# Kernel tuning notes

Hardware: AMD Instinct MI355X
Metric: run time of the kernel (lower is better)

## Reference

```python
import jax, jax.numpy as jnp
import numpy as np

N_NODES = 100000
N_EDGES = 1600000
D_FEAT = 128
HIDDEN = 128
N_CLASSES = 40


def setup_inputs() -> dict:
    key = jax.random.key(0)
    ks = jax.random.split(key, 8)
    s = 1.0 / np.sqrt(HIDDEN)
    return {
        "x": jax.random.normal(ks[0], (N_NODES, D_FEAT), dtype=jnp.float32),
        "edge_index": jax.random.randint(ks[1], (2, N_EDGES), 0, N_NODES, dtype=jnp.int64),
        "w1a": jax.random.normal(ks[2], (D_FEAT, HIDDEN), dtype=jnp.float32) * s,
        "b1a": jnp.zeros((HIDDEN,), dtype=jnp.float32),
        "w1b": jax.random.normal(ks[3], (HIDDEN, HIDDEN), dtype=jnp.float32) * s,
        "b1b": jnp.zeros((HIDDEN,), dtype=jnp.float32),
        "w2a": jax.random.normal(ks[4], (HIDDEN, HIDDEN), dtype=jnp.float32) * s,
        "b2a": jnp.zeros((HIDDEN,), dtype=jnp.float32),
        "w2b": jax.random.normal(ks[5], (HIDDEN, HIDDEN), dtype=jnp.float32) * s,
        "b2b": jnp.zeros((HIDDEN,), dtype=jnp.float32),
        "wfc": jax.random.normal(ks[6], (HIDDEN, N_CLASSES), dtype=jnp.float32) * s,
        "bfc": jnp.zeros((N_CLASSES,), dtype=jnp.float32),
    }


def _gin_conv(x, src, dst, wa, ba, wb, bb):
    # sum-aggregate neighbor features: agg[i] = sum_{(j->i) in E} x[j]
    agg = jax.ops.segment_sum(x[src], dst, num_segments=N_NODES)
    h = x + agg  # eps = 0 (PyG GINConv default)
    h = jax.nn.relu(h @ wa + ba)
    return h @ wb + bb


def reference(x, edge_index, w1a, b1a, w1b, b1b, w2a, b2a, w2b, b2b, wfc, bfc):
    src, dst = edge_index[0], edge_index[1]
    h = jax.nn.relu(_gin_conv(x, src, dst, w1a, b1a, w1b, b1b))
    # dropout is identity at inference
    h = jax.nn.relu(_gin_conv(h, src, dst, w2a, b2a, w2b, b2b))
    logits = h @ wfc + bfc
    return jax.nn.log_softmax(logits, axis=1)
```

## Files before the change

### kernel.cpp

```cpp
#include <hip/hip_runtime.h>
#include <hip/hip_bf16.h>

#define NNODES 100000
#define NEDGES 1600000
#define DF 128
#define NC 40
#define NCP 48
#define NB 196
#define CH 4096
#define MLP_BLOCKS 512
#define MLP_WAVES (MLP_BLOCKS * 4)
#define ZROW NNODES
#define CVT_BLOCKS 6250
#define WPREP_N (4 * 16384 + NCP * 128 + 512 + NC + 512)
#define WPREP_BLOCKS ((WPREP_N + 255) / 256)
#define NEB ((NEDGES + CH - 1) / CH)

typedef __bf16 bf16x8 __attribute__((ext_vector_type(8)));
typedef float f32x4 __attribute__((ext_vector_type(4)));
typedef float f32x2 __attribute__((ext_vector_type(2)));

__device__ __forceinline__ unsigned short f2bf(float f) {
    unsigned int u = __builtin_bit_cast(unsigned int, f);
    u = (u + 0x7FFFu + ((u >> 16) & 1u)) >> 16;
    return (unsigned short)u;
}
__device__ __forceinline__ float bf2f(unsigned short s) {
    unsigned int u = ((unsigned int)s) << 16;
    return __builtin_bit_cast(float, u);
}
__device__ __forceinline__ float bfLo(unsigned int u) {
    return __builtin_bit_cast(float, u << 16);
}
__device__ __forceinline__ float bfHi(unsigned int u) {
    return __builtin_bit_cast(float, u & 0xFFFF0000u);
}
__device__ __forceinline__ f32x2 up2(unsigned int u) {
    return (f32x2){bfLo(u), bfHi(u)};
}

__global__ void k_detect(const unsigned int* __restrict__ ei32,
                         const unsigned int* __restrict__ x32,
                         int* __restrict__ flags,
                         int* __restrict__ binCnt) {
    __shared__ unsigned int rOr[256];
    __shared__ int rCnt[256];
    for (int i = threadIdx.x; i < NB; i += 256) binCnt[i] = 0;
    unsigned int o = 0; int c = 0;
    for (int i = threadIdx.x; i < 1024; i += 256) o |= ei32[2 * i + 1];
    for (int i = threadIdx.x; i < 4096; i += 256) {
        unsigned int e = (x32[i] >> 7) & 0xFFu;
        c += (e >= 100u && e <= 140u) ? 1 : 0;
    }
    rOr[threadIdx.x] = o; rCnt[threadIdx.x] = c;
    __syncthreads();
    for (int s = 128; s; s >>= 1) {
        if ((int)threadIdx.x < s) {
            rOr[threadIdx.x] |= rOr[threadIdx.x + s];
            rCnt[threadIdx.x] += rCnt[threadIdx.x + s];
        }
        __syncthreads();
    }
    if (threadIdx.x == 0) {
        flags[0] = (rOr[0] == 0u) ? 1 : 0;
        flags[1] = (rCnt[0] > 2457) ? 1 : 0;
    }
}

__device__ __forceinline__ int ldIdx(const void* ei, int flag64, int i) {
    return flag64 ? (int)((const long long*)ei)[i] : ((const int*)ei)[i];
}

__global__ __launch_bounds__(256) void k_prep(const void* __restrict__ src,
                                              const void* w1a, const void* w1b,
                                              const void* w2a, const void* w2b,
                                              const void* wfc,
                                              const void* b1a, const void* b1b,
                                              const void* b2a, const void* b2b,
                                              const void* bfc,
                                              const void* __restrict__ ei,
                                              const int* __restrict__ flags,
                                              unsigned short* __restrict__ dst,
                                              unsigned short* __restrict__ wAll,
                                              float* __restrict__ bAll,
                                              unsigned short* __restrict__ pad0,
                                              unsigned short* __restrict__ pad1,
                                              int* __restrict__ binCnt) {
    int bf = flags[1];
    if (blockIdx.x < CVT_BLOCKS) {
        int i = blockIdx.x * 256 + threadIdx.x;
        if (bf) {
            ((uint4*)dst)[i] = ((const uint4*)src)[i];
        } else {
            uint4 a = ((const uint4*)src)[2 * i];
            uint4 b = ((const uint4*)src)[2 * i + 1];
            auto pk = [](unsigned int lo, unsigned int hi) -> unsigned int {
                return ((unsigned int)f2bf(__builtin_bit_cast(float, hi)) << 16) |
                       f2bf(__builtin_bit_cast(float, lo));
            };
            uint4 r;
            r.x = pk(a.x, a.y);
            r.y = pk(a.z, a.w);
            r.z = pk(b.x, b.y);
            r.w = pk(b.z, b.w);
            ((uint4*)dst)[i] = r;
        }
        return;
    }
    if (blockIdx.x >= CVT_BLOCKS + WPREP_BLOCKS) {
        __shared__ int l[NB];
        int t = threadIdx.x;
        int f64 = flags[0];
        for (int i = t; i < NB; i += 256) l[i] = 0;
        __syncthreads();
        int base = (blockIdx.x - CVT_BLOCKS - WPREP_BLOCKS) * CH;
#pragma unroll
        for (int k = 0; k < CH / 256; k++) {
            int e = base + k * 256 + t;
            if (e < NEDGES) atomicAdd(&l[ldIdx(ei, f64, NEDGES + e) >> 9], 1);
        }
        __syncthreads();
        for (int i = t; i < NB; i += 256)
            if (l[i]) atomicAdd(&binCnt[i], l[i]);
        return;
    }
    int idx = (blockIdx.x - CVT_BLOCKS) * 256 + threadIdx.x;
    auto ldf = [&](const void* p, int i) -> float {
        return bf ? bf2f(((const unsigned short*)p)[i]) : ((const float*)p)[i];
    };
    if (idx < 65536) {
        int wi = idx >> 14, r = idx & 16383;
        int n = r >> 7, k = r & 127;
        const void* s = (wi == 0) ? w1a : (wi == 1) ? w1b : (wi == 2) ? w2a : w2b;
        wAll[idx] = f2bf(ldf(s, k * 128 + n));
    } else if (idx < 65536 + NCP * 128) {
        int r = idx - 65536;
        int n = r >> 7, k = r & 127;
        wAll[idx] = (n < NC) ? f2bf(ldf(wfc, k * NC + n)) : (unsigned short)0;
    } else if (idx < 65536 + NCP * 128 + 512 + NC) {
        int r = idx - (65536 + NCP * 128);
        const void* s; int i;
        if (r < 128)      { s = b1a; i = r; }
        else if (r < 256) { s = b1b; i = r - 128; }
        else if (r < 384) { s = b2a; i = r - 256; }
        else if (r < 512) { s = b2b; i = r - 384; }
        else              { s = bfc; i = r - 512; }
        bAll[r] = ldf(s, i);
    } else if (idx < 65536 + NCP * 128 + 512 + NC + 256) {
        pad0[idx - (65536 + NCP * 128 + 512 + NC)] = 0;
    } else if (idx < 65536 + NCP * 128 + 512 + NC + 512) {
        pad1[idx - (65536 + NCP * 128 + 512 + NC + 256)] = 0;
    }
}

__global__ __launch_bounds__(256) void k_binscan(const int* __restrict__ binCnt,
                                                 int* __restrict__ binOfs,
                                                 int* __restrict__ binCur) {
    __shared__ int sh[256];
    int t = threadIdx.x;
    int v = (t < NB) ? binCnt[t] : 0;
    sh[t] = v;
    __syncthreads();
    for (int off = 1; off < 256; off <<= 1) {
        int x = (t >= off) ? sh[t - off] : 0;
        __syncthreads();
        sh[t] += x;
        __syncthreads();
    }
    if (t < NB) {
        binOfs[t + 1] = sh[t];
        binCur[t] = sh[t] - v;
    }
    if (t == 0) binOfs[0] = 0;
}

__global__ __launch_bounds__(256) void k_binscatter(const void* __restrict__ ei,
                                                    const int* __restrict__ flags,
                                                    int* __restrict__ binCur,
                                                    int2* __restrict__ ebin) {
    __shared__ int lcnt[NB], lbase[NB], lofs[NB];
    int t = threadIdx.x;
    int f64 = flags[0];
    for (int i = t; i < NB; i += 256) lcnt[i] = 0;
    __syncthreads();
    int base = blockIdx.x * CH;
    int2 ed[CH / 256];
    int bn[CH / 256];
#pragma unroll
    for (int k = 0; k < CH / 256; k++) {
        int e = base + k * 256 + t;
        if (e < NEDGES) {
            ed[k].x = ldIdx(ei, f64, e);
            ed[k].y = ldIdx(ei, f64, NEDGES + e);
            bn[k] = ed[k].y >> 9;
            atomicAdd(&lcnt[bn[k]], 1);
        } else bn[k] = -1;
    }
    __syncthreads();
    if (t < NB) {
        int c = lcnt[t];
        lbase[t] = c ? atomicAdd(&binCur[t], c) : 0;
        lofs[t] = 0;
    }
    __syncthreads();
#pragma unroll
    for (int k = 0; k < CH / 256; k++) {
        if (bn[k] >= 0) {
            int p = lbase[bn[k]] + atomicAdd(&lofs[bn[k]], 1);
            ebin[p] = ed[k];
        }
    }
}

__global__ __launch_bounds__(256) void k_binfill(const int2* __restrict__ ebin,
                                                 const int* __restrict__ binOfs,
                                                 int* __restrict__ rowptr,
                                                 int* __restrict__ perm) {
    __shared__ int deg[512], lptr[512], ssum[256];
    int b = blockIdx.x, t = threadIdx.x;
    int n0 = b << 9;
    int nn = NNODES - n0; if (nn > 512) nn = 512;
    int e0 = binOfs[b], e1 = binOfs[b + 1];
    deg[t] = 0; deg[t + 256] = 0;
    __syncthreads();
    for (int e = e0 + t; e < e1; e += 256)
        atomicAdd(&deg[ebin[e].y - n0], 1);
    __syncthreads();
    int d0 = deg[2 * t], d1 = deg[2 * t + 1];
    int s = d0 + d1;
    ssum[t] = s;
    __syncthreads();
    for (int off = 1; off < 256; off <<= 1) {
        int x = (t >= off) ? ssum[t - off] : 0;
        __syncthreads();
        ssum[t] += x;
        __syncthreads();
    }
    int ex = ssum[t] - s;
    lptr[2 * t] = ex;
    lptr[2 * t + 1] = ex + d0;
    if (2 * t < nn)     rowptr[n0 + 2 * t] = e0 + ex;
    if (2 * t + 1 < nn) rowptr[n0 + 2 * t + 1] = e0 + ex + d0;
    if (b == NB - 1 && t == 0) rowptr[NNODES] = e1;
    deg[2 * t] = 0; deg[2 * t + 1] = 0;
    __syncthreads();
    for (int e = e0 + t; e < e1; e += 256) {
        int2 ed = ebin[e];
        int d = ed.y - n0;
        int pos = e0 + lptr[d] + atomicAdd(&deg[d], 1);
        perm[pos] = ed.x;
    }
}

__device__ __forceinline__ void accu(f32x2* acc, uint4 u) {
    acc[0] += up2(u.x);
    acc[1] += up2(u.y);
    acc[2] += up2(u.z);
    acc[3] += up2(u.w);
}

template <int S>
__device__ __forceinline__ void gslots(const int* __restrict__ perm, const uint4* __restrict__ F,
                                       int j, int je, int g, int c, f32x2* acc) {
    int pm[S];
#pragma unroll
    for (int k = 0; k < S; k++) pm[k] = perm[j + 4 * k + g];
#pragma unroll
    for (int k = 0; k < S; k++)
        if (j + 4 * k + g >= je) pm[k] = ZROW;
    uint4 u[S];
#pragma unroll
    for (int k = 0; k < S; k++) u[k] = F[pm[k] * 16 + c];
#pragma unroll
    for (int k = 0; k < S; k++) accu(acc, u[k]);
}

__global__ __launch_bounds__(256) void k_gather(const unsigned short* __restrict__ feat,
                                                const unsigned short* __restrict__ x,
                                                const int* __restrict__ rowptr,
                                                const int* __restrict__ perm,
                                                unsigned short* __restrict__ out) {
    int wave = threadIdx.x >> 6, lane = threadIdx.x & 63;
    int i = blockIdx.x * 4 + wave;
    int g = lane >> 4, c = lane & 15;
    const uint4* F = (const uint4*)feat;

    uint4 xv = ((const uint4*)x)[i * 16 + c];
    int jb = rowptr[i], je = rowptr[i + 1];

    f32x2 acc[4];
#pragma unroll
    for (int k = 0; k < 4; k++) acc[k] = (f32x2){0.f, 0.f};

    int j = jb;
    while (je - j > 24) {
        int s0 = perm[j + g], s1 = perm[j + 4 + g];
        int s2 = perm[j + 8 + g], s3 = perm[j + 12 + g];
        uint4 u0 = F[s0 * 16 + c];
        uint4 u1 = F[s1 * 16 + c];
        uint4 u2 = F[s2 * 16 + c];
        uint4 u3 = F[s3 * 16 + c];
        accu(acc, u0); accu(acc, u1); accu(acc, u2); accu(acc, u3);
        j += 16;
    }
    int deg = je - j;
    if (deg > 16)      gslots<6>(perm, F, j, je, g, c, acc);
    else if (deg > 8)  gslots<4>(perm, F, j, je, g, c, acc);
    else if (deg > 0)  gslots<2>(perm, F, j, je, g, c, acc);

#pragma unroll
    for (int k = 0; k < 4; k++) {
        acc[k][0] += __shfl_xor(acc[k][0], 16);
        acc[k][1] += __shfl_xor(acc[k][1], 16);
        acc[k][0] += __shfl_xor(acc[k][0], 32);
        acc[k][1] += __shfl_xor(acc[k][1], 32);
    }

    acc[0] += up2(xv.x);
    acc[1] += up2(xv.y);
    acc[2] += up2(xv.z);
    acc[3] += up2(xv.w);

    if (g == 0) {
        uint4 r;
        r.x = ((unsigned int)f2bf(acc[0][1]) << 16) | f2bf(acc[0][0]);
        r.y = ((unsigned int)f2bf(acc[1][1]) << 16) | f2bf(acc[1][0]);
        r.z = ((unsigned int)f2bf(acc[2][1]) << 16) | f2bf(acc[2][0]);
        r.w = ((unsigned int)f2bf(acc[3][1]) << 16) | f2bf(acc[3][0]);
        ((uint4*)out)[i * 16 + c] = r;
    }
}

template <bool DOFC>
__global__ __launch_bounds__(256, 2) void k_mlp_lds(const unsigned short* __restrict__ A,
                                                    const unsigned short* __restrict__ WaT,
                                                    const float* __restrict__ ba,
                                                    const unsigned short* __restrict__ WbT,
                                                    const float* __restrict__ bb,
                                                    const unsigned short* __restrict__ WfcT,
                                                    const float* __restrict__ bfc,
                                                    const int* __restrict__ flags,
                                                    unsigned short* __restrict__ outH,
                                                    void* __restrict__ outFC) {
    __shared__ __align__(16) unsigned short sWa[16384];
    __shared__ __align__(16) unsigned short sWb[16384];
    __shared__ __align__(16) unsigned short sT[4][2048];

    int wave = threadIdx.x >> 6, lane = threadIdx.x & 63;
    int gw = blockIdx.x * 4 + wave;
    int m = lane & 15, quad = lane >> 4;
    unsigned short* T = sT[wave];

    {
        const uint4* Wa4 = (const uint4*)WaT;
        const uint4* Wb4 = (const uint4*)WbT;
        uint4* sA4 = (uint4*)sWa;
        uint4* sB4 = (uint4*)sWb;
        for (int idx = (int)threadIdx.x; idx < 2048; idx += 256) {
            int n = idx >> 4, kc = idx & 15;
            int d = (n << 4) | (kc ^ (n & 15));
            sA4[d] = Wa4[idx];
            sB4[d] = Wb4[idx];
        }
    }

    float bva[8], bvb[8];
#pragma unroll
    for (int nt = 0; nt < 8; nt++) { bva[nt] = ba[nt * 16 + m]; bvb[nt] = bb[nt * 16 + m]; }

    bf16x8 wf[3][4];
    float fv0 = 0.f, fv1 = 0.f, fv2 = 0.f;
    bool valid2 = (m < 8);
    int obf = 0;
    if (DOFC) {
#pragma unroll
        for (int nt = 0; nt < 3; nt++) {
            const unsigned short* Bf = WfcT + (nt * 16 + m) * DF + quad * 8;
#pragma unroll
            for (int ks = 0; ks < 4; ks++) wf[nt][ks] = *(const bf16x8*)(Bf + ks * 32);
        }
        fv0 = bfc[m]; fv1 = bfc[16 + m];
        fv2 = valid2 ? bfc[32 + m] : 0.f;
        obf = flags[1];
    }
    __syncthreads();

    for (int tile = gw; tile < NNODES / 16; tile += MLP_WAVES) {
        int r0 = tile * 16;
        const unsigned short* Ab = A + (r0 + m) * DF + quad * 8;
        bf16x8 a[4];
#pragma unroll
        for (int ks = 0; ks < 4; ks++) a[ks] = *(const bf16x8*)(Ab + ks * 32);

        f32x4 acc[8];
#pragma unroll
        for (int nt = 0; nt < 8; nt++) acc[nt] = (f32x4){0.f, 0.f, 0.f, 0.f};
#pragma unroll
        for (int nt = 0; nt < 8; nt++) {
#pragma unroll
            for (int ks = 0; ks < 4; ks++) {
                bf16x8 w = *(const bf16x8*)&sWa[((nt * 16 + m) << 7) | ((((ks << 2) + quad) ^ m) << 3)];
                acc[nt] = __builtin_amdgcn_mfma_f32_16x16x32_bf16(a[ks], w, acc[nt], 0, 0, 0);
            }
        }

#pragma unroll
        for (int nt = 0; nt < 8; nt++)
#pragma unroll
            for (int reg = 0; reg < 4; reg++) {
                float v = acc[nt][reg] + bva[nt];
                if (v < 0.f) v = 0.f;
                int row = quad * 4 + reg, col = nt * 16 + m;
                T[(row << 7) | ((((col >> 3) ^ row) & 15) << 3) | (col & 7)] = f2bf(v);
            }

        bf16x8 a2[4];
#pragma unroll
        for (int ks = 0; ks < 4; ks++)
            a2[ks] = *(const bf16x8*)&T[(m << 7) | ((((ks << 2) + quad) ^ m) << 3)];
#pragma unroll
        for (int nt = 0; nt < 8; nt++) acc[nt] = (f32x4){0.f, 0.f, 0.f, 0.f};
#pragma unroll
        for (int nt = 0; nt < 8; nt++) {
#pragma unroll
            for (int ks = 0; ks < 4; ks++) {
                bf16x8 w = *(const bf16x8*)&sWb[((nt * 16 + m) << 7) | ((((ks << 2) + quad) ^ m) << 3)];
                acc[nt] = __builtin_amdgcn_mfma_f32_16x16x32_bf16(a2[ks], w, acc[nt], 0, 0, 0);
            }
        }

        if (!DOFC) {
#pragma unroll
            for (int nt = 0; nt < 8; nt++)
#pragma unroll
                for (int reg = 0; reg < 4; reg++) {
                    float v = acc[nt][reg] + bvb[nt];
                    if (v < 0.f) v = 0.f;
                    int row = quad * 4 + reg, col = nt * 16 + m;
                    T[(row << 7) | ((((col >> 3) ^ row) & 15) << 3) | (col & 7)] = f2bf(v);
                }
            int r2 = lane >> 3, c8 = lane & 7;
            const uint4* T4 = (const uint4*)T;
            uint4* O4 = (uint4*)(outH + (size_t)r0 * DF);
#pragma unroll
            for (int half = 0; half < 2; half++) {
                int row = r2 + half * 8;
#pragma unroll
                for (int lin = 0; lin < 2; lin++) {
                    int ch = c8 + lin * 8;
                    uint4 v = T4[(row << 4) | (ch ^ row)];
                    O4[row * 16 + ch] = v;
                }
            }
        } else {
#pragma unroll
            for (int nt = 0; nt < 8; nt++)
#pragma unroll
                for (int reg = 0; reg < 4; reg++) {
                    float v = acc[nt][reg] + bvb[nt];
                    if (v < 0.f) v = 0.f;
                    int row = quad * 4 + reg, col = nt * 16 + m;
                    T[(row << 7) | ((((col >> 3) ^ row) & 15) << 3) | (col & 7)] = f2bf(v);
                }
            bf16x8 a3[4];
#pragma unroll
            for (int ks = 0; ks < 4; ks++)
                a3[ks] = *(const bf16x8*)&T[(m << 7) | ((((ks << 2) + quad) ^ m) << 3)];
            f32x4 fa[3];
#pragma unroll
            for (int nt = 0; nt < 3; nt++) fa[nt] = (f32x4){0.f, 0.f, 0.f, 0.f};
#pragma unroll
            for (int nt = 0; nt < 3; nt++)
#pragma unroll
                for (int ks = 0; ks < 4; ks++)
                    fa[nt] = __builtin_amdgcn_mfma_f32_16x16x32_bf16(a3[ks], wf[nt][ks], fa[nt], 0, 0, 0);

            float ov[3][4];
#pragma unroll
            for (int reg = 0; reg < 4; reg++) {
                float v0 = fa[0][reg] + fv0;
                float v1 = fa[1][reg] + fv1;
                float v2 = valid2 ? (fa[2][reg] + fv2) : -3.0e38f;
                float mx = fmaxf(fmaxf(v0, v1), v2);
#pragma unroll
                for (int off = 1; off < 16; off <<= 1) mx = fmaxf(mx, __shfl_xor(mx, off, 16));
                float e = __expf(v0 - mx) + __expf(v1 - mx) + (valid2 ? __expf(v2 - mx) : 0.f);
#pragma unroll
                for (int off = 1; off < 16; off <<= 1) e += __shfl_xor(e, off, 16);
                float l = mx + __logf(e);
                ov[0][reg] = v0 - l;
                ov[1][reg] = v1 - l;
                ov[2][reg] = v2 - l;
            }
            if (obf) {
                unsigned short* Ts = T;
#pragma unroll
                for (int reg = 0; reg < 4; reg++) {
                    int row = quad * 4 + reg;
                    Ts[row * 40 + m] = f2bf(ov[0][reg]);
                    Ts[row * 40 + 16 + m] = f2bf(ov[1][reg]);
                    if (valid2) Ts[row * 40 + 32 + m] = f2bf(ov[2][reg]);
                }
                const uint4* T4 = (const uint4*)Ts;
                uint4* O4 = (uint4*)((unsigned short*)outFC + (size_t)r0 * NC);
#pragma unroll
                for (int it = 0; it < 2; it++) {
                    int idx = it * 64 + lane;
                    if (idx < 80) O4[idx] = T4[idx];
                }
            } else {
                float* Tf = (float*)T;
#pragma unroll
                for (int reg = 0; reg < 4; reg++) {
                    int row = quad * 4 + reg;
                    Tf[row * 40 + m] = ov[0][reg];
                    Tf[row * 40 + 16 + m] = ov[1][reg];
                    if (valid2) Tf[row * 40 + 32 + m] = ov[2][reg];
                }
                const uint4* T4 = (const uint4*)Tf;
                uint4* O4 = (uint4*)((float*)outFC + (size_t)r0 * NC);
#pragma unroll
                for (int it = 0; it < 3; it++) {
                    int idx = it * 64 + lane;
                    if (idx < 160) O4[idx] = T4[idx];
                }
            }
        }
    }
}

extern "C" void kernel_launch(void* const* d_in, const int* in_sizes, int n_in,
                              void* d_out, int out_size, void* d_ws, size_t ws_size,
                              hipStream_t stream) {
    const void* x   = d_in[0];
    const void* ei  = d_in[1];
    const void* w1a = d_in[2];
    const void* b1a = d_in[3];
    const void* w1b = d_in[4];
    const void* b1b = d_in[5];
    const void* w2a = d_in[6];
    const void* b2a = d_in[7];
    const void* w2b = d_in[8];
    const void* b2b = d_in[9];
    const void* wfc = d_in[10];
    const void* bfc = d_in[11];

    char* ws = (char*)d_ws;
    size_t off = 0;
    auto alloc = [&](size_t bytes) {
        void* p = ws + off;
        off += (bytes + 255) & ~(size_t)255;
        return p;
    };
    unsigned short* B0    = (unsigned short*)alloc((size_t)(NNODES + 1) * DF * 2);
    unsigned short* B1    = (unsigned short*)alloc((size_t)(NNODES + 1) * DF * 2);
    int2*           ebin  = (int2*)alloc((size_t)NEDGES * 8);
    int*            perm  = (int*)alloc((size_t)(NEDGES + 64) * 4);
    int*            rowptr= (int*)alloc((size_t)(NNODES + 1) * 4);
    int*            binCnt= (int*)alloc(NB * 4);
    int*            binOfs= (int*)alloc((NB + 1) * 4);
    int*            binCur= (int*)alloc(NB * 4);
    int*            flags = (int*)alloc(256);
    unsigned short* wAll  = (unsigned short*)alloc((4 * 16384 + NCP * 128) * 2);
    float*          bAll  = (float*)alloc((512 + NC) * 4);

    unsigned short* w1aT = wAll;
    unsigned short* w1bT = wAll + 16384;
    unsigned short* w2aT = wAll + 32768;
    unsigned short* w2bT = wAll + 49152;
    unsigned short* wfcT = wAll + 65536;
    float* b1af = bAll;
    float* b1bf = bAll + 128;
    float* b2af = bAll + 256;
    float* b2bf = bAll + 384;
    float* bfcf = bAll + 512;

    k_detect<<<1, 256, 0, stream>>>((const unsigned int*)ei, (const unsigned int*)x, flags, binCnt);
    int prepGrid = CVT_BLOCKS + WPREP_BLOCKS + NEB;
    k_prep<<<prepGrid, 256, 0, stream>>>(x, w1a, w1b, w2a, w2b, wfc,
                                         b1a, b1b, b2a, b2b, bfc, ei,
                                         flags, B0, wAll, bAll,
                                         B0 + (size_t)NNODES * DF,
                                         B1 + (size_t)NNODES * DF,
                                         binCnt);

    k_binscan<<<1, 256, 0, stream>>>(binCnt, binOfs, binCur);
    k_binscatter<<<NEB, 256, 0, stream>>>(ei, flags, binCur, ebin);
    k_binfill<<<NB, 256, 0, stream>>>(ebin, binOfs, rowptr, perm);

    const int gatherGrid = NNODES / 4;

    k_gather<<<gatherGrid, 256, 0, stream>>>(B0, B0, rowptr, perm, B1);
    k_mlp_lds<false><<<MLP_BLOCKS, 256, 0, stream>>>(B1, w1aT, b1af, w1bT, b1bf,
                                                     nullptr, nullptr, flags, B0, nullptr);

    k_gather<<<gatherGrid, 256, 0, stream>>>(B0, B0, rowptr, perm, B1);
    k_mlp_lds<true><<<MLP_BLOCKS, 256, 0, stream>>>(B1, w2aT, b2af, w2bT, b2bf,
                                                    wfcT, bfcf, flags, nullptr, d_out);
}
```

Measured before the change: 336.4 us.

## Fuse neighbor gather-aggregation into the MLP kernel via per-wave LDS tile

Removes the separate gather kernel and has each MLP wave aggregate the neighbor sums for its own 16-row tile, two rows at a time, writing the bf16 result into a swizzled LDS tile that feeds the MFMA A operand directly. This drops one global write and one global read of the aggregated feature matrix per layer, plus two kernel launches. The cost is that the gather now runs at the MLP kernel's low occupancy (512 blocks, launch_bounds 256,2), so there is less parallelism available to hide random-access latency. The tail path now always issues 6 slots per row instead of picking the slot count by degree.

```diff
diff --git a/kernel.cpp b/kernel.cpp
--- a/kernel.cpp
+++ b/kernel.cpp
@@ -259,89 +259,19 @@
     acc[3] += up2(u.w);
 }
 
-template <int S>
-__device__ __forceinline__ void gslots(const int* __restrict__ perm, const uint4* __restrict__ F,
-                                       int j, int je, int g, int c, f32x2* acc) {
-    int pm[S];
-#pragma unroll
-    for (int k = 0; k < S; k++) pm[k] = perm[j + 4 * k + g];
-#pragma unroll
-    for (int k = 0; k < S; k++)
-        if (j + 4 * k + g >= je) pm[k] = ZROW;
-    uint4 u[S];
-#pragma unroll
-    for (int k = 0; k < S; k++) u[k] = F[pm[k] * 16 + c];
-#pragma unroll
-    for (int k = 0; k < S; k++) accu(acc, u[k]);
-}
-
-__global__ __launch_bounds__(256) void k_gather(const unsigned short* __restrict__ feat,
-                                                const unsigned short* __restrict__ x,
-                                                const int* __restrict__ rowptr,
-                                                const int* __restrict__ perm,
-                                                unsigned short* __restrict__ out) {
-    int wave = threadIdx.x >> 6, lane = threadIdx.x & 63;
-    int i = blockIdx.x * 4 + wave;
-    int g = lane >> 4, c = lane & 15;
-    const uint4* F = (const uint4*)feat;
-
-    uint4 xv = ((const uint4*)x)[i * 16 + c];
-    int jb = rowptr[i], je = rowptr[i + 1];
-
-    f32x2 acc[4];
-#pragma unroll
-    for (int k = 0; k < 4; k++) acc[k] = (f32x2){0.f, 0.f};
-
-    int j = jb;
-    while (je - j > 24) {
-        int s0 = perm[j + g], s1 = perm[j + 4 + g];
-        int s2 = perm[j + 8 + g], s3 = perm[j + 12 + g];
-        uint4 u0 = F[s0 * 16 + c];
-        uint4 u1 = F[s1 * 16 + c];
-        uint4 u2 = F[s2 * 16 + c];
-        uint4 u3 = F[s3 * 16 + c];
-        accu(acc, u0); accu(acc, u1); accu(acc, u2); accu(acc, u3);
-        j += 16;
-    }
-    int deg = je - j;
-    if (deg > 16)      gslots<6>(perm, F, j, je, g, c, acc);
-    else if (deg > 8)  gslots<4>(perm, F, j, je, g, c, acc);
-    else if (deg > 0)  gslots<2>(perm, F, j, je, g, c, acc);
-
-#pragma unroll
-    for (int k = 0; k < 4; k++) {
-        acc[k][0] += __shfl_xor(acc[k][0], 16);
-        acc[k][1] += __shfl_xor(acc[k][1], 16);
-        acc[k][0] += __shfl_xor(acc[k][0], 32);
-        acc[k][1] += __shfl_xor(acc[k][1], 32);
-    }
-
-    acc[0] += up2(xv.x);
-    acc[1] += up2(xv.y);
-    acc[2] += up2(xv.z);
-    acc[3] += up2(xv.w);
-
-    if (g == 0) {
-        uint4 r;
-        r.x = ((unsigned int)f2bf(acc[0][1]) << 16) | f2bf(acc[0][0]);
-        r.y = ((unsigned int)f2bf(acc[1][1]) << 16) | f2bf(acc[1][0]);
-        r.z = ((unsigned int)f2bf(acc[2][1]) << 16) | f2bf(acc[2][0]);
-        r.w = ((unsigned int)f2bf(acc[3][1]) << 16) | f2bf(acc[3][0]);
-        ((uint4*)out)[i * 16 + c] = r;
-    }
-}
-
 template <bool DOFC>
-__global__ __launch_bounds__(256, 2) void k_mlp_lds(const unsigned short* __restrict__ A,
-                                                    const unsigned short* __restrict__ WaT,
-                                                    const float* __restrict__ ba,
-                                                    const unsigned short* __restrict__ WbT,
-                                                    const float* __restrict__ bb,
-                                                    const unsigned short* __restrict__ WfcT,
-                                                    const float* __restrict__ bfc,
-                                                    const int* __restrict__ flags,
-                                                    unsigned short* __restrict__ outH,
-                                                    void* __restrict__ outFC) {
+__global__ __launch_bounds__(256, 2) void k_gmlp(const unsigned short* __restrict__ feat,
+                                                 const int* __restrict__ rowptr,
+                                                 const int* __restrict__ perm,
+                                                 const unsigned short* __restrict__ WaT,
+                                                 const float* __restrict__ ba,
+                                                 const unsigned short* __restrict__ WbT,
+                                                 const float* __restrict__ bb,
+                                                 const unsigned short* __restrict__ WfcT,
+                                                 const float* __restrict__ bfc,
+                                                 const int* __restrict__ flags,
+                                                 unsigned short* __restrict__ outH,
+                                                 void* __restrict__ outFC) {
     __shared__ __align__(16) unsigned short sWa[16384];
     __shared__ __align__(16) unsigned short sWb[16384];
     __shared__ __align__(16) unsigned short sT[4][2048];
@@ -349,7 +279,9 @@
     int wave = threadIdx.x >> 6, lane = threadIdx.x & 63;
     int gw = blockIdx.x * 4 + wave;
     int m = lane & 15, quad = lane >> 4;
+    int g = quad, c = m;
     unsigned short* T = sT[wave];
+    const uint4* F = (const uint4*)feat;
 
     {
         const uint4* Wa4 = (const uint4*)WaT;
@@ -387,10 +319,91 @@
 
     for (int tile = gw; tile < NNODES / 16; tile += MLP_WAVES) {
         int r0 = tile * 16;
-        const unsigned short* Ab = A + (r0 + m) * DF + quad * 8;
+
+        for (int p = 0; p < 8; p++) {
+            int i0 = r0 + 2 * p;
+            uint4 xv0 = F[(size_t)i0 * 16 + c];
+            uint4 xv1 = F[(size_t)(i0 + 1) * 16 + c];
+            int jb0 = rowptr[i0], mid = rowptr[i0 + 1], je1 = rowptr[i0 + 2];
+
+            f32x2 a0[4], a1[4];
+#pragma unroll
+            for (int k = 0; k < 4; k++) { a0[k] = (f32x2){0.f, 0.f}; a1[k] = (f32x2){0.f, 0.f}; }
+
+            int j0 = jb0, je0 = mid, j1 = mid;
+            while (je0 - j0 > 24) {
+                int s0 = perm[j0 + g], s1 = perm[j0 + 4 + g];
+                int s2 = perm[j0 + 8 + g], s3 = perm[j0 + 12 + g];
+                uint4 u0 = F[s0 * 16 + c], u1 = F[s1 * 16 + c];
+                uint4 u2 = F[s2 * 16 + c], u3 = F[s3 * 16 + c];
+                accu(a0, u0); accu(a0, u1); accu(a0, u2); accu(a0, u3);
+                j0 += 16;
+            }
+            while (je1 - j1 > 24) {
+                int s0 = perm[j1 + g], s1 = perm[j1 + 4 + g];
+                int s2 = perm[j1 + 8 + g], s3 = perm[j1 + 12 + g];
+                uint4 u0 = F[s0 * 16 + c], u1 = F[s1 * 16 + c];
+                uint4 u2 = F[s2 * 16 + c], u3 = F[s3 * 16 + c];
+                accu(a1, u0); accu(a1, u1); accu(a1, u2); accu(a1, u3);
+                j1 += 16;
+            }
+
+            int pm0[6], pm1[6];
+#pragma unroll
+            for (int k = 0; k < 6; k++) pm0[k] = perm[j0 + 4 * k + g];
+#pragma unroll
+            for (int k = 0; k < 6; k++) pm1[k] = perm[j1 + 4 * k + g];
+#pragma unroll
+            for (int k = 0; k < 6; k++) if (j0 + 4 * k + g >= je0) pm0[k] = ZROW;
+#pragma unroll
+            for (int k = 0; k < 6; k++) if (j1 + 4 * k + g >= je1) pm1[k] = ZROW;
+            uint4 u0[6], u1[6];
+#pragma unroll
+            for (int k = 0; k < 6; k++) u0[k] = F[pm0[k] * 16 + c];
+#pragma unroll
+            for (int k = 0; k < 6; k++) u1[k] = F[pm1[k] * 16 + c];
+#pragma unroll
+            for (int k = 0; k < 6; k++) accu(a0, u0[k]);
+#pragma unroll
+            for (int k = 0; k < 6; k++) accu(a1, u1[k]);
+
+#pragma unroll
+            for (int k = 0; k < 4; k++) {
+                a0[k][0] += __shfl_xor(a0[k][0], 16);
+                a0[k][1] += __shfl_xor(a0[k][1], 16);
+                a0[k][0] += __shfl_xor(a0[k][0], 32);
+                a0[k][1] += __shfl_xor(a0[k][1], 32);
+                a1[k][0] += __shfl_xor(a1[k][0], 16);
+                a1[k][1] += __shfl_xor(a1[k][1], 16);
+                a1[k][0] += __shfl_xor(a1[k][0], 32);
+                a1[k][1] += __shfl_xor(a1[k][1], 32);
+            }
+            a0[0] += up2(xv0.x); a0[1] += up2(xv0.y); a0[2] += up2(xv0.z); a0[3] += up2(xv0.w);
+            a1[0] += up2(xv1.x); a1[1] += up2(xv1.y); a1[2] += up2(xv1.z); a1[3] += up2(xv1.w);
+
+            if (g == 0) {
+                int row = 2 * p;
+                uint4 r;
+                r.x = ((unsigned int)f2bf(a0[0][1]) << 16) | f2bf(a0[0][0]);
+                r.y = ((unsigned int)f2bf(a0[1][1]) << 16) | f2bf(a0[1][0]);
+                r.z = ((unsigned int)f2bf(a0[2][1]) << 16) | f2bf(a0[2][0]);
+                r.w = ((unsigned int)f2bf(a0[3][1]) << 16) | f2bf(a0[3][0]);
+                ((uint4*)T)[(row << 4) | (c ^ row)] = r;
+            } else if (g == 1) {
+                int row = 2 * p + 1;
+                uint4 r;
+                r.x = ((unsigned int)f2bf(a1[0][1]) << 16) | f2bf(a1[0][0]);
+                r.y = ((unsigned int)f2bf(a1[1][1]) << 16) | f2bf(a1[1][0]);
+                r.z = ((unsigned int)f2bf(a1[2][1]) << 16) | f2bf(a1[2][0]);
+                r.w = ((unsigned int)f2bf(a1[3][1]) << 16) | f2bf(a1[3][0]);
+                ((uint4*)T)[(row << 4) | (c ^ row)] = r;
+            }
+        }
+
         bf16x8 a[4];
 #pragma unroll
-        for (int ks = 0; ks < 4; ks++) a[ks] = *(const bf16x8*)(Ab + ks * 32);
+        for (int ks = 0; ks < 4; ks++)
+            a[ks] = *(const bf16x8*)&T[(m << 7) | ((((ks << 2) + quad) ^ m) << 3)];
 
         f32x4 acc[8];
 #pragma unroll
@@ -588,13 +601,11 @@
     k_binscatter<<<NEB, 256, 0, stream>>>(ei, flags, binCur, ebin);
     k_binfill<<<NB, 256, 0, stream>>>(ebin, binOfs, rowptr, perm);
 
-    const int gatherGrid = NNODES / 4;
-
-    k_gather<<<gatherGrid, 256, 0, stream>>>(B0, B0, rowptr, perm, B1);
-    k_mlp_lds<false><<<MLP_BLOCKS, 256, 0, stream>>>(B1, w1aT, b1af, w1bT, b1bf,
-                                                     nullptr, nullptr, flags, B0, nullptr);
-
-    k_gather<<<gatherGrid, 256, 0, stream>>>(B0, B0, rowptr, perm, B1);
-    k_mlp_lds<true><<<MLP_BLOCKS, 256, 0, stream>>>(B1, w2aT, b2af, w2bT, b2bf,
-                                                    wfcT, bfcf, flags, nullptr, d_out);
-}
+    k_gmlp<false><<<MLP_BLOCKS, 256, 0, stream>>>(B0, rowptr, perm,
+                                                  w1aT, b1af, w1bT, b1bf,
+                                                  nullptr, nullptr, flags, B1, nullptr);
+
+    k_gmlp<true><<<MLP_BLOCKS, 256, 0, stream>>>(B1, rowptr, perm,
+                                                 w2aT, b2af, w2bT, b2bf,
+                                                 wfcT, bfcf, flags, nullptr, d_out);
+}
```

Result: slower. 350.8 us (+4.3%).
